# Kernel optimization log

Hardware: AMD Instinct MI355X
Metric: run time of the kernel (lower is better)

The kernel has to match this reference:

```python
import jax, jax.numpy as jnp
import numpy as np

B, L, D, H = 4, 2048, 1024, 16
HD = D // H


def setup_inputs() -> dict:
    key = jax.random.key(0)
    k1, k2, k3 = jax.random.split(key, 3)
    # xavier_uniform bounds for Linear(d, 3d) and Linear(d, d)
    b_qkv = float(np.sqrt(6.0 / (D + 3 * D)))
    b_out = float(np.sqrt(6.0 / (D + D)))
    x = jax.random.normal(k1, (B, L, D), dtype=jnp.float32)
    W_qkv = jax.random.uniform(k2, (3 * D, D), dtype=jnp.float32, minval=-b_qkv, maxval=b_qkv)
    W_out = jax.random.uniform(k3, (D, D), dtype=jnp.float32, minval=-b_out, maxval=b_out)
    return {"x": x, "W_qkv": W_qkv, "W_out": W_out}


def reference(x, W_qkv, W_out):
    b, l, d = x.shape
    # fused QKV projection: [B,L,3d] -> [3,B,H,L,Hd]
    qkv = (x @ W_qkv.T).reshape(b, l, 3, H, HD).transpose(2, 0, 3, 1, 4)
    q, k, v = qkv[0], qkv[1], qkv[2]
    # naive causal attention: full [B,H,L,L] score matrix, as in the original
    scores = jnp.einsum('bhqd,bhkd->bhqk', q, k) / (HD ** 0.5)
    mask = jnp.tril(jnp.ones((l, l), dtype=bool))  # causal mask recomputed per call
    scores = jnp.where(mask, scores, -jnp.inf)
    attn = jax.nn.softmax(scores, axis=-1)
    ctx = jnp.einsum('bhqk,bhkd->bhqd', attn, v)          # [B,H,L,Hd]
    ctx = ctx.transpose(0, 2, 1, 3).reshape(b, l, d)       # [B,L,d]
    return ctx @ W_out.T
```

## Files before the change

### kernel.cpp

```cpp
#include <hip/hip_runtime.h>

#define BB 4
#define LL 2048
#define DD 1024
#define HH 16
#define HD 64

typedef __attribute__((ext_vector_type(8))) short s16x8;
typedef __attribute__((ext_vector_type(4))) short s16x4;
typedef __attribute__((ext_vector_type(4))) float f32x4;

#define SCALE_LOG2E 0.18033688011112042f

__device__ __forceinline__ short f2bf(float f) {
  union { float f; unsigned u; } c;
  c.f = f;
  return (short)((c.u + 0x7fffu + ((c.u >> 16) & 1u)) >> 16);
}

__device__ __forceinline__ void cp16(const void* g, void* l) {
  __builtin_amdgcn_global_load_lds(
      (const __attribute__((address_space(1))) void*)g,
      (__attribute__((address_space(3))) void*)l, 16, 0, 0);
}

__global__ __launch_bounds__(256) void f2b_kernel(const float* __restrict__ in,
                                                  short* __restrict__ out, int n4) {
  int i = blockIdx.x * blockDim.x + threadIdx.x;
  if (i >= n4) return;
  float4 v = ((const float4*)in)[i];
  s16x4 o;
  o[0] = f2bf(v.x);
  o[1] = f2bf(v.y);
  o[2] = f2bf(v.z);
  o[3] = f2bf(v.w);
  ((s16x4*)out)[i] = o;
}

template <int MODE>
__global__ __launch_bounds__(256) void gemm_bt(const short* __restrict__ A,
                                               const short* __restrict__ Bm,
                                               int K, int N,
                                               short* __restrict__ qo,
                                               short* __restrict__ ko,
                                               short* __restrict__ vo,
                                               float* __restrict__ fo) {
  __shared__ __align__(16) short As[2][128 * 32];
  __shared__ __align__(16) short Bs[2][128 * 32];
  const int tid = threadIdx.x;
  const int m0 = blockIdx.y * 128, n0 = blockIdx.x * 128;
  const int wave = tid >> 6, lane = tid & 63;
  const int quad = lane >> 4, c16 = lane & 15;
  const int wr = (wave >> 1) * 64, wc = (wave & 1) * 64;

  f32x4 zero = {0.f, 0.f, 0.f, 0.f};
  f32x4 acc[4][4];
#pragma unroll
  for (int i = 0; i < 4; i++)
#pragma unroll
    for (int j = 0; j < 4; j++) acc[i][j] = zero;

  const int row1 = tid >> 2, seg = (tid & 3) * 8;
  const short* Ag = A + (size_t)(m0 + row1) * K + seg;
  const short* Bg = Bm + (size_t)(n0 + row1) * K + seg;

  auto stage = [&](int k0, int bi) {
    cp16(Ag + k0, As[bi] + wave * 512);
    cp16(Ag + (size_t)64 * K + k0, As[bi] + 2048 + wave * 512);
    cp16(Bg + k0, Bs[bi] + wave * 512);
    cp16(Bg + (size_t)64 * K + k0, Bs[bi] + 2048 + wave * 512);
  };

  stage(0, 0);
  __syncthreads();
  const int T = K >> 5;
  for (int t = 0; t < T; t++) {
    if (t + 1 < T) stage((t + 1) * 32, (t + 1) & 1);
    const short* Asb = As[t & 1];
    const short* Bsb = Bs[t & 1];
    s16x8 af[4], bf[4];
#pragma unroll
    for (int i = 0; i < 4; i++)
      af[i] = *(const s16x8*)&Asb[(wr + i * 16 + c16) * 32 + quad * 8];
#pragma unroll
    for (int j = 0; j < 4; j++)
      bf[j] = *(const s16x8*)&Bsb[(wc + j * 16 + c16) * 32 + quad * 8];
#pragma unroll
    for (int i = 0; i < 4; i++)
#pragma unroll
      for (int j = 0; j < 4; j++)
        acc[i][j] = __builtin_amdgcn_mfma_f32_16x16x32_bf16(af[i], bf[j], acc[i][j], 0, 0, 0);
    __syncthreads();
  }

  if (MODE == 0) {
#pragma unroll
    for (int j = 0; j < 4; j++) {
      const int gn = n0 + wc + j * 16 + c16;
      const int which = gn >> 10;
      const int h = (gn >> 6) & 15;
      const int hd = gn & 63;
      if (which == 2) {
#pragma unroll
        for (int i = 0; i < 4; i++)
#pragma unroll
          for (int r = 0; r < 4; r++) {
            const int gm = m0 + wr + i * 16 + quad * 4 + r;
            const int b = gm >> 11, l = gm & 2047;
            vo[((size_t)((b << 4) + h) * HD + hd) * LL + l] = f2bf(acc[i][j][r]);
          }
      } else {
        short* dst = which == 0 ? qo : ko;
        const float sc = which == 0 ? SCALE_LOG2E : 1.0f;
#pragma unroll
        for (int i = 0; i < 4; i++)
#pragma unroll
          for (int r = 0; r < 4; r++) {
            const int gm = m0 + wr + i * 16 + quad * 4 + r;
            const int b = gm >> 11, l = gm & 2047;
            dst[((size_t)((b << 4) + h) * LL + l) * HD + hd] = f2bf(acc[i][j][r] * sc);
          }
      }
    }
  } else {
#pragma unroll
    for (int i = 0; i < 4; i++)
#pragma unroll
      for (int r = 0; r < 4; r++) {
        const int gm = m0 + wr + i * 16 + quad * 4 + r;
#pragma unroll
        for (int j = 0; j < 4; j++) {
          const int gn = n0 + wc + j * 16 + c16;
          fo[(size_t)gm * N + gn] = acc[i][j][r];
        }
      }
  }
}

__global__ __launch_bounds__(256) void attn_kernel(const short* __restrict__ Qb,
                                                   const short* __restrict__ Kb,
                                                   const short* __restrict__ Vtb,
                                                   short* __restrict__ Cb) {
  const int pi = blockIdx.x;
  const int bh = blockIdx.y;
  const int tid = threadIdx.x;
  const int wave = tid >> 6, lane = tid & 63;
  const int quad = lane >> 4, c16 = lane & 15;
  const int sw = c16 & 7;
  const size_t base = (size_t)bh * LL * HD;
  const short* Q = Qb + base;
  const short* K = Kb + base;
  const short* Vt = Vtb + base;

  __shared__ __align__(16) short Ks[2][128 * 64];
  __shared__ __align__(16) short Vs[2][64 * 128];

  const f32x4 zero = {0.f, 0.f, 0.f, 0.f};
  const s16x4 ones = {(short)0x3F80, (short)0x3F80, (short)0x3F80, (short)0x3F80};

  const int k_r = lane >> 3, k_c = lane & 7;
  const int v_r = lane >> 4, v_c = lane & 15;
  auto stage = [&](int kb, int bi) {
#pragma unroll
    for (int i = 0; i < 4; i++) {
      const int gk = i * 32 + wave * 8 + k_r;
      cp16(K + (size_t)(kb + gk) * HD + ((k_c ^ (gk & 7)) * 8),
           &Ks[bi][i * 2048 + wave * 512]);
      const int gv = i * 16 + wave * 4 + v_r;
      cp16(Vt + (size_t)gv * LL + kb + ((v_c ^ (gv & 15)) * 8),
           &Vs[bi][i * 2048 + wave * 512]);
    }
  };

  auto pack4 = [&](const float* p) {
    union { float f; unsigned u; } a0, a1, a2, a3;
    a0.f = p[0]; a1.f = p[1]; a2.f = p[2]; a3.f = p[3];
    union { s16x4 v; unsigned u[2]; } r;
    r.u[0] = __builtin_amdgcn_perm(a1.u, a0.u, 0x07060302u);
    r.u[1] = __builtin_amdgcn_perm(a3.u, a2.u, 0x07060302u);
    return r.v;
  };

  for (int phase = 0; phase < 2; phase++) {
    const int qg = phase == 0 ? (15 - pi) : pi;
    const int qw = qg * 128 + wave * 32;
    const int tiles = qg + 1;

    s16x8 qf[2][2];
#pragma unroll
    for (int h = 0; h < 2; h++)
#pragma unroll
      for (int s = 0; s < 2; s++)
        qf[h][s] = *(const s16x8*)(Q + (size_t)(qw + h * 16 + c16) * HD + s * 32 + quad * 8);

    f32x4 o[2][4];
#pragma unroll
    for (int h = 0; h < 2; h++)
#pragma unroll
      for (int j = 0; j < 4; j++) o[h][j] = zero;
    f32x4 ol[2] = {zero, zero};

    stage(0, 0);
    __syncthreads();

    for (int t = 0; t < tiles; t++) {
      const int kb = t * 128;
      if (t + 1 < tiles) stage(kb + 128, (t + 1) & 1);
      const short* Kt = &Ks[t & 1][0];
      const short* Vv = &Vs[t & 1][0];

      const int D0 = qw - kb, D1 = D0 + 16;
      const int jm0 = D0 < 0 ? 0 : min((D0 >> 4) + 1, 8);
      const int jm1 = D1 < 0 ? 0 : min((D1 >> 4) + 1, 8);
      const int jb0 = D0 >> 4, jb1 = D1 >> 4;

#pragma unroll
      for (int j = 0; j < 8; j++) {
        if (j >= jm1) continue;
        s16x8 kf0 = *(const s16x8*)&Kt[(j * 16 + c16) * 64 + ((quad ^ sw) * 8)];
        s16x8 kf1 = *(const s16x8*)&Kt[(j * 16 + c16) * 64 + (((4 + quad) ^ sw) * 8)];
        s16x4 va[4];
#pragma unroll
        for (int j4 = 0; j4 < 4; j4++)
          va[j4] = *(const s16x4*)&Vv[(j4 * 16 + c16) * 128 +
                                      (((2 * j + (quad >> 1)) ^ c16) * 8) + (quad & 1) * 4];
        {
          f32x4 s = __builtin_amdgcn_mfma_f32_16x16x32_bf16(kf0, qf[1][0], zero, 0, 0, 0);
          s = __builtin_amdgcn_mfma_f32_16x16x32_bf16(kf1, qf[1][1], s, 0, 0, 0);
          float p[4];
#pragma unroll
          for (int r = 0; r < 4; r++) p[r] = exp2f(s[r]);
          if (j == jb1) {
            const int thr = c16 + D1 - j * 16 - quad * 4;
#pragma unroll
            for (int r = 0; r < 4; r++)
              if (r > thr) p[r] = 0.f;
          }
          s16x4 pb = pack4(p);
          ol[1] = __builtin_amdgcn_mfma_f32_16x16x16bf16_1k(ones, pb, ol[1], 0, 0, 0);
#pragma unroll
          for (int j4 = 0; j4 < 4; j4++)
            o[1][j4] = __builtin_amdgcn_mfma_f32_16x16x16bf16_1k(va[j4], pb, o[1][j4], 0, 0, 0);
        }
        if (j < jm0) {
          f32x4 s = __builtin_amdgcn_mfma_f32_16x16x32_bf16(kf0, qf[0][0], zero, 0, 0, 0);
          s = __builtin_amdgcn_mfma_f32_16x16x32_bf16(kf1, qf[0][1], s, 0, 0, 0);
          float p[4];
#pragma unroll
          for (int r = 0; r < 4; r++) p[r] = exp2f(s[r]);
          if (j == jb0) {
            const int thr = c16 + D0 - j * 16 - quad * 4;
#pragma unroll
            for (int r = 0; r < 4; r++)
              if (r > thr) p[r] = 0.f;
          }
          s16x4 pb = pack4(p);
          ol[0] = __builtin_amdgcn_mfma_f32_16x16x16bf16_1k(ones, pb, ol[0], 0, 0, 0);
#pragma unroll
          for (int j4 = 0; j4 < 4; j4++)
            o[0][j4] = __builtin_amdgcn_mfma_f32_16x16x16bf16_1k(va[j4], pb, o[0][j4], 0, 0, 0);
        }
      }

      __syncthreads();
    }

    const int b = bh >> 4, h2 = bh & 15;
#pragma unroll
    for (int h = 0; h < 2; h++) {
      const float inv = 1.0f / ol[h][0];
      const int q = qw + h * 16 + c16;
#pragma unroll
      for (int j4 = 0; j4 < 4; j4++) {
        s16x4 ov;
#pragma unroll
        for (int r = 0; r < 4; r++) ov[r] = f2bf(o[h][j4][r] * inv);
        *(s16x4*)&Cb[(size_t)(b * LL + q) * DD + h2 * HD + j4 * 16 + quad * 4] = ov;
      }
    }
  }
}

extern "C" void kernel_launch(void* const* d_in, const int* in_sizes, int n_in,
                              void* d_out, int out_size, void* d_ws, size_t ws_size,
                              hipStream_t stream) {
  const float* x = (const float*)d_in[0];
  const float* wqkv = (const float*)d_in[1];
  const float* wout = (const float*)d_in[2];
  float* out = (float*)d_out;

  const size_t NX = (size_t)BB * LL * DD;
  short* xb = (short*)d_ws;
  short* wqkvb = xb + NX;
  short* woutb = wqkvb + (size_t)3 * DD * DD;
  short* qb = woutb + (size_t)DD * DD;
  short* kb = qb + NX;
  short* vb = kb + NX;
  short* cb = vb + NX;

  f2b_kernel<<<dim3((unsigned)(NX / 4 / 256)), 256, 0, stream>>>(x, xb, (int)(NX / 4));
  f2b_kernel<<<dim3(3 * DD * DD / 4 / 256), 256, 0, stream>>>(wqkv, wqkvb, 3 * DD * DD / 4);
  f2b_kernel<<<dim3(DD * DD / 4 / 256), 256, 0, stream>>>(wout, woutb, DD * DD / 4);

  gemm_bt<0><<<dim3(3 * DD / 128, BB * LL / 128), 256, 0, stream>>>(
      xb, wqkvb, DD, 3 * DD, qb, kb, vb, nullptr);
  attn_kernel<<<dim3(8, BB * HH), 256, 0, stream>>>(qb, kb, vb, cb);
  gemm_bt<1><<<dim3(DD / 128, BB * LL / 128), 256, 0, stream>>>(
      cb, woutb, DD, DD, nullptr, nullptr, nullptr, out);
}
```

Measured before the change: 288.0 us.

## Double attention block to 512 threads with one 16-row query strip per wave

```diff
diff --git a/kernel.cpp b/kernel.cpp
--- a/kernel.cpp
+++ b/kernel.cpp
@@ -102,13 +102,14 @@
       const int hd = gn & 63;
       if (which == 2) {
 #pragma unroll
-        for (int i = 0; i < 4; i++)
-#pragma unroll
-          for (int r = 0; r < 4; r++) {
-            const int gm = m0 + wr + i * 16 + quad * 4 + r;
-            const int b = gm >> 11, l = gm & 2047;
-            vo[((size_t)((b << 4) + h) * HD + hd) * LL + l] = f2bf(acc[i][j][r]);
-          }
+        for (int i = 0; i < 4; i++) {
+          const int gm = m0 + wr + i * 16 + quad * 4;
+          const int b = gm >> 11, l = gm & 2047;
+          s16x4 vv;
+#pragma unroll
+          for (int r = 0; r < 4; r++) vv[r] = f2bf(acc[i][j][r]);
+          *(s16x4*)&vo[((size_t)((b << 4) + h) * HD + hd) * LL + l] = vv;
+        }
       } else {
         short* dst = which == 0 ? qo : ko;
         const float sc = which == 0 ? SCALE_LOG2E : 1.0f;
@@ -137,10 +138,10 @@
   }
 }
 
-__global__ __launch_bounds__(256) void attn_kernel(const short* __restrict__ Qb,
-                                                   const short* __restrict__ Kb,
-                                                   const short* __restrict__ Vtb,
-                                                   short* __restrict__ Cb) {
+__global__ __launch_bounds__(512, 4) void attn_kernel(const short* __restrict__ Qb,
+                                                      const short* __restrict__ Kb,
+                                                      const short* __restrict__ Vtb,
+                                                      short* __restrict__ Cb) {
   const int pi = blockIdx.x;
   const int bh = blockIdx.y;
   const int tid = threadIdx.x;
@@ -160,15 +161,15 @@
 
   const int k_r = lane >> 3, k_c = lane & 7;
   const int v_r = lane >> 4, v_c = lane & 15;
+  const int ksw = (k_c ^ k_r) * 8;
+  const int vsw = (v_c ^ ((wave * 4 + v_r) & 15)) * 8;
   auto stage = [&](int kb, int bi) {
 #pragma unroll
-    for (int i = 0; i < 4; i++) {
-      const int gk = i * 32 + wave * 8 + k_r;
-      cp16(K + (size_t)(kb + gk) * HD + ((k_c ^ (gk & 7)) * 8),
-           &Ks[bi][i * 2048 + wave * 512]);
-      const int gv = i * 16 + wave * 4 + v_r;
-      cp16(Vt + (size_t)gv * LL + kb + ((v_c ^ (gv & 15)) * 8),
-           &Vs[bi][i * 2048 + wave * 512]);
+    for (int i = 0; i < 2; i++) {
+      const int gk = i * 64 + wave * 8 + k_r;
+      cp16(K + (size_t)(kb + gk) * HD + ksw, &Ks[bi][(i * 64 + wave * 8) * 64]);
+      const int gv = i * 32 + wave * 4 + v_r;
+      cp16(Vt + (size_t)gv * LL + kb + vsw, &Vs[bi][(i * 32 + wave * 4) * 128]);
     }
   };
 
@@ -183,22 +184,18 @@
 
   for (int phase = 0; phase < 2; phase++) {
     const int qg = phase == 0 ? (15 - pi) : pi;
-    const int qw = qg * 128 + wave * 32;
+    const int qw = qg * 128 + wave * 16;
     const int tiles = qg + 1;
 
-    s16x8 qf[2][2];
-#pragma unroll
-    for (int h = 0; h < 2; h++)
-#pragma unroll
-      for (int s = 0; s < 2; s++)
-        qf[h][s] = *(const s16x8*)(Q + (size_t)(qw + h * 16 + c16) * HD + s * 32 + quad * 8);
-
-    f32x4 o[2][4];
-#pragma unroll
-    for (int h = 0; h < 2; h++)
-#pragma unroll
-      for (int j = 0; j < 4; j++) o[h][j] = zero;
-    f32x4 ol[2] = {zero, zero};
+    s16x8 qf[2];
+#pragma unroll
+    for (int s = 0; s < 2; s++)
+      qf[s] = *(const s16x8*)(Q + (size_t)(qw + c16) * HD + s * 32 + quad * 8);
+
+    f32x4 o[4];
+#pragma unroll
+    for (int j4 = 0; j4 < 4; j4++) o[j4] = zero;
+    f32x4 ol = zero;
 
     stage(0, 0);
     __syncthreads();
@@ -209,14 +206,13 @@
       const short* Kt = &Ks[t & 1][0];
       const short* Vv = &Vs[t & 1][0];
 
-      const int D0 = qw - kb, D1 = D0 + 16;
-      const int jm0 = D0 < 0 ? 0 : min((D0 >> 4) + 1, 8);
-      const int jm1 = D1 < 0 ? 0 : min((D1 >> 4) + 1, 8);
-      const int jb0 = D0 >> 4, jb1 = D1 >> 4;
+      const int D = qw - kb;
+      const int jm = min((D >> 4) + 1, 8);
+      const int jb = D >> 4;
 
 #pragma unroll
       for (int j = 0; j < 8; j++) {
-        if (j >= jm1) continue;
+        if (j >= jm) continue;
         s16x8 kf0 = *(const s16x8*)&Kt[(j * 16 + c16) * 64 + ((quad ^ sw) * 8)];
         s16x8 kf1 = *(const s16x8*)&Kt[(j * 16 + c16) * 64 + (((4 + quad) ^ sw) * 8)];
         s16x4 va[4];
@@ -224,59 +220,36 @@
         for (int j4 = 0; j4 < 4; j4++)
           va[j4] = *(const s16x4*)&Vv[(j4 * 16 + c16) * 128 +
                                       (((2 * j + (quad >> 1)) ^ c16) * 8) + (quad & 1) * 4];
-        {
-          f32x4 s = __builtin_amdgcn_mfma_f32_16x16x32_bf16(kf0, qf[1][0], zero, 0, 0, 0);
-          s = __builtin_amdgcn_mfma_f32_16x16x32_bf16(kf1, qf[1][1], s, 0, 0, 0);
-          float p[4];
-#pragma unroll
-          for (int r = 0; r < 4; r++) p[r] = exp2f(s[r]);
-          if (j == jb1) {
-            const int thr = c16 + D1 - j * 16 - quad * 4;
-#pragma unroll
-            for (int r = 0; r < 4; r++)
-              if (r > thr) p[r] = 0.f;
-          }
-          s16x4 pb = pack4(p);
-          ol[1] = __builtin_amdgcn_mfma_f32_16x16x16bf16_1k(ones, pb, ol[1], 0, 0, 0);
-#pragma unroll
-          for (int j4 = 0; j4 < 4; j4++)
-            o[1][j4] = __builtin_amdgcn_mfma_f32_16x16x16bf16_1k(va[j4], pb, o[1][j4], 0, 0, 0);
+        f32x4 s = __builtin_amdgcn_mfma_f32_16x16x32_bf16(kf0, qf[0], zero, 0, 0, 0);
+        s = __builtin_amdgcn_mfma_f32_16x16x32_bf16(kf1, qf[1], s, 0, 0, 0);
+        float p[4];
+#pragma unroll
+        for (int r = 0; r < 4; r++) p[r] = __builtin_amdgcn_exp2f(s[r]);
+        if (j == jb) {
+          const int thr = c16 + D - j * 16 - quad * 4;
+#pragma unroll
+          for (int r = 0; r < 4; r++)
+            if (r > thr) p[r] = 0.f;
         }
-        if (j < jm0) {
-          f32x4 s = __builtin_amdgcn_mfma_f32_16x16x32_bf16(kf0, qf[0][0], zero, 0, 0, 0);
-          s = __builtin_amdgcn_mfma_f32_16x16x32_bf16(kf1, qf[0][1], s, 0, 0, 0);
-          float p[4];
-#pragma unroll
-          for (int r = 0; r < 4; r++) p[r] = exp2f(s[r]);
-          if (j == jb0) {
-            const int thr = c16 + D0 - j * 16 - quad * 4;
-#pragma unroll
-            for (int r = 0; r < 4; r++)
-              if (r > thr) p[r] = 0.f;
-          }
-          s16x4 pb = pack4(p);
-          ol[0] = __builtin_amdgcn_mfma_f32_16x16x16bf16_1k(ones, pb, ol[0], 0, 0, 0);
-#pragma unroll
-          for (int j4 = 0; j4 < 4; j4++)
-            o[0][j4] = __builtin_amdgcn_mfma_f32_16x16x16bf16_1k(va[j4], pb, o[0][j4], 0, 0, 0);
-        }
+        s16x4 pb = pack4(p);
+        ol = __builtin_amdgcn_mfma_f32_16x16x16bf16_1k(ones, pb, ol, 0, 0, 0);
+#pragma unroll
+        for (int j4 = 0; j4 < 4; j4++)
+          o[j4] = __builtin_amdgcn_mfma_f32_16x16x16bf16_1k(va[j4], pb, o[j4], 0, 0, 0);
       }
 
       __syncthreads();
     }
 
     const int b = bh >> 4, h2 = bh & 15;
-#pragma unroll
-    for (int h = 0; h < 2; h++) {
-      const float inv = 1.0f / ol[h][0];
-      const int q = qw + h * 16 + c16;
-#pragma unroll
-      for (int j4 = 0; j4 < 4; j4++) {
-        s16x4 ov;
-#pragma unroll
-        for (int r = 0; r < 4; r++) ov[r] = f2bf(o[h][j4][r] * inv);
-        *(s16x4*)&Cb[(size_t)(b * LL + q) * DD + h2 * HD + j4 * 16 + quad * 4] = ov;
-      }
+    const float inv = 1.0f / ol[0];
+    const int q = qw + c16;
+#pragma unroll
+    for (int j4 = 0; j4 < 4; j4++) {
+      s16x4 ov;
+#pragma unroll
+      for (int r = 0; r < 4; r++) ov[r] = f2bf(o[j4][r] * inv);
+      *(s16x4*)&Cb[(size_t)(b * LL + q) * DD + h2 * HD + j4 * 16 + quad * 4] = ov;
     }
   }
 }
@@ -304,7 +277,7 @@
 
   gemm_bt<0><<<dim3(3 * DD / 128, BB * LL / 128), 256, 0, stream>>>(
       xb, wqkvb, DD, 3 * DD, qb, kb, vb, nullptr);
-  attn_kernel<<<dim3(8, BB * HH), 256, 0, stream>>>(qb, kb, vb, cb);
+  attn_kernel<<<dim3(8, BB * HH), 512, 0, stream>>>(qb, kb, vb, cb);
   gemm_bt<1><<<dim3(DD / 128, BB * LL / 128), 256, 0, stream>>>(
       cb, woutb, DD, DD, nullptr, nullptr, nullptr, out);
 }
```

After: 253.0 us. -12.1%, faster.
